# Performance work log

Measured on AMD Instinct MI355X. Metric: run time of the kernel, lower is better.

## Reference

```python
import jax, jax.numpy as jnp
import numpy as np

B, NQ, NK = 8, 1024, 1024
DQ = DK = DV = 512
H = 8
DS = DV // H
EPS = 1e-4
MAX_ITER = 3
SQRT_V = DV ** 0.25  # sqrt(sqrt(dim_V))


def setup_inputs() -> dict:
    key = jax.random.key(0)
    ks = jax.random.split(key, 8)
    s = 0.02
    return {
        "Q": jax.random.normal(ks[0], (B, NQ, DQ), jnp.float32),
        "K": jax.random.normal(ks[1], (B, NK, DK), jnp.float32),
        "Wq": jax.random.normal(ks[2], (DV, DQ), jnp.float32) * s,
        "bq": jnp.zeros((DV,), jnp.float32),
        "Wk": jax.random.normal(ks[3], (DV, DK), jnp.float32) * s,
        "bk": jnp.zeros((DV,), jnp.float32),
        "Wv": jax.random.normal(ks[4], (DV, DK), jnp.float32) * s,
        "bv": jnp.zeros((DV,), jnp.float32),
        "Wo": jax.random.normal(ks[5], (DV, DV), jnp.float32) * s,
        "bo": jnp.zeros((DV,), jnp.float32),
    }


def _split_heads(x):
    # torch.cat(x.split(ds, 2), 0): head-major stacking along batch
    b, n, _ = x.shape
    return x.reshape(b, n, H, DS).transpose(2, 0, 1, 3).reshape(H * b, n, DS)


def _merge_heads(x, b):
    # torch.cat(x.split(b, 0), 2): inverse of _split_heads
    _, n, ds = x.shape
    return x.reshape(H, b, n, ds).transpose(1, 2, 0, 3).reshape(b, n, H * ds)


def _sinkhorn_plan(x, y):
    # x: [M, P1, d], y: [M, P2, d]; cost = pairwise Euclidean (p=2) distance.
    x2 = jnp.sum(x * x, axis=-1)[:, :, None]
    y2 = jnp.sum(y * y, axis=-1)[:, None, :]
    C = jnp.sqrt(jnp.maximum(x2 + y2 - 2.0 * jnp.einsum("mid,mjd->mij", x, y), 0.0))
    m, p1, p2 = C.shape
    log_a = -jnp.log(jnp.float32(p1))  # uniform marginals
    log_b = -jnp.log(jnp.float32(p2))
    u = jnp.zeros((m, p1), C.dtype)
    v = jnp.zeros((m, p2), C.dtype)
    for _ in range(MAX_ITER):  # fixed small iteration count (max_iter=3)
        u = EPS * (log_a - jax.scipy.special.logsumexp((v[:, None, :] - C) / EPS, axis=2))
        v = EPS * (log_b - jax.scipy.special.logsumexp((u[:, :, None] - C) / EPS, axis=1))
    # transport plan P: [M, P1, P2]
    return jnp.exp((u[:, :, None] + v[:, None, :] - C) / EPS)


def reference(Q, K, Wq, bq, Wk, bk, Wv, bv, Wo, bo):
    q = Q @ Wq.T + bq            # [B, NQ, DV]
    k = K @ Wk.T + bk            # [B, NK, DV]
    v = K @ Wv.T + bv            # [B, NK, DV]
    b = Q.shape[0]
    q_, k_, v_ = _split_heads(q), _split_heads(k), _split_heads(v)  # [H*B, N, DS]
    A = _sinkhorn_plan(q_ / SQRT_V, k_ / SQRT_V)                    # [H*B, NQ, NK]
    O = _merge_heads(q_ + jnp.einsum("mij,mjd->mid", A, v_), b)     # [B, NQ, DV]
    return O + jax.nn.relu(O @ Wo.T + bo)
```

## Files before the change

### kernel.cpp

```cpp
#include <hip/hip_runtime.h>
#include <hip/hip_bf16.h>
#include <math.h>

#define NB 8
#define NN 1024
#define ND 512
#define NH 8
#define NDS 64
#define NM 64
#define LOG_A (-6.93147180559945f)
#define SQRT_V 4.75682846001088f
#define INV_SQRT_V 0.210224103813429f
#define INV_EPS 10000.0f
#define L2E  1.44269504088896f
#define LN2F 0.693147180559945f
#define IEL2 14426.9504088896f

#define SPLIT_ELEMS ((size_t)NM * NN * NDS)
#define W_ELEMS     ((size_t)ND * ND)
#define UV_FLOATS   ((size_t)NM * NN)

typedef unsigned short u16;
typedef unsigned int   u32;
typedef __attribute__((ext_vector_type(8))) short bf16x8;
typedef __attribute__((ext_vector_type(4))) float f32x4;

#define MFMA16(a,b,c) __builtin_amdgcn_mfma_f32_16x16x32_bf16(a,b,c,0,0,0)

__device__ __forceinline__ u16 f2bf_t(float x) {
  return (u16)(__float_as_uint(x) >> 16);
}
__device__ __forceinline__ float bf2f(u16 h) {
  return __uint_as_float(((u32)h) << 16);
}
__device__ __forceinline__ float fast_sqrt(float x) {
  float r;
  asm("v_sqrt_f32 %0, %1" : "=v"(r) : "v"(x));
  return r;
}
__device__ __forceinline__ float fast_exp2(float x) {
  float r;
  asm("v_exp_f32 %0, %1" : "=v"(r) : "v"(x));
  return r;
}
__device__ __forceinline__ float max3f(float a, float b, float c) {
  float r;
  asm("v_max3_f32 %0, %1, %2, %3" : "=v"(r) : "v"(a), "v"(b), "v"(c));
  return r;
}

__global__ __launch_bounds__(256) void k_split(
    const float* __restrict__ X, u16* __restrict__ hi, u16* __restrict__ lo)
{
  const size_t i = ((size_t)blockIdx.x * 256 + threadIdx.x) * 4;
  float4 v = *(const float4*)&X[i];
  const float* vp = (const float*)&v;
  u16 h[4], l[4];
#pragma unroll
  for (int j = 0; j < 4; ++j) {
    h[j] = f2bf_t(vp[j]);
    l[j] = f2bf_t(vp[j] - bf2f(h[j]));
  }
  uint2 ph, pl;
  ph.x = (u32)h[0] | ((u32)h[1] << 16);
  ph.y = (u32)h[2] | ((u32)h[3] << 16);
  pl.x = (u32)l[0] | ((u32)l[1] << 16);
  pl.y = (u32)l[2] | ((u32)l[3] << 16);
  *(uint2*)&hi[i] = ph;
  *(uint2*)&lo[i] = pl;
}

__global__ __launch_bounds__(256) void k_proj_mfma(
    const u16* __restrict__ Xh, const u16* __restrict__ Xl,
    const u16* __restrict__ Wh, const u16* __restrict__ Wl,
    const float* __restrict__ bias, u16* __restrict__ oh,
    u16* __restrict__ ol, u16* __restrict__ oT,
    float* __restrict__ nrm, float scale, int mode)
{
  __shared__ __align__(16) u16 Xhs[64][72];
  __shared__ __align__(16) u16 Xls[64][72];
  __shared__ __align__(16) u16 Whs[64][72];
  __shared__ __align__(16) u16 Wls[64][72];
  const int t = threadIdx.x;
  const int r0 = blockIdx.x * 64;
  const int h  = blockIdx.y;
  const int c0 = h * 64;
  const int w = t >> 6, l = t & 63;
  const int c = l & 15, kg = l >> 4;
  const int srow = t >> 2;
  const int skoff = (t & 3) * 16;

  f32x4 acc[4];
#pragma unroll
  for (int cf = 0; cf < 4; ++cf) acc[cf] = (f32x4){0.f, 0.f, 0.f, 0.f};

  for (int kt = 0; kt < 8; ++kt) {
    const int k0 = kt * 64;
    __syncthreads();
    {
      const u16* gxh = &Xh[(size_t)(r0 + srow) * ND + k0 + skoff];
      const u16* gxl = &Xl[(size_t)(r0 + srow) * ND + k0 + skoff];
      const u16* gwh = &Wh[(size_t)(c0 + srow) * ND + k0 + skoff];
      const u16* gwl = &Wl[(size_t)(c0 + srow) * ND + k0 + skoff];
      *(bf16x8*)&Xhs[srow][skoff]     = *(const bf16x8*)gxh;
      *(bf16x8*)&Xhs[srow][skoff + 8] = *(const bf16x8*)(gxh + 8);
      *(bf16x8*)&Xls[srow][skoff]     = *(const bf16x8*)gxl;
      *(bf16x8*)&Xls[srow][skoff + 8] = *(const bf16x8*)(gxl + 8);
      *(bf16x8*)&Whs[srow][skoff]     = *(const bf16x8*)gwh;
      *(bf16x8*)&Whs[srow][skoff + 8] = *(const bf16x8*)(gwh + 8);
      *(bf16x8*)&Wls[srow][skoff]     = *(const bf16x8*)gwl;
      *(bf16x8*)&Wls[srow][skoff + 8] = *(const bf16x8*)(gwl + 8);
    }
    __syncthreads();
#pragma unroll
    for (int ks = 0; ks < 2; ++ks) {
      bf16x8 Ah = *(const bf16x8*)&Xhs[w * 16 + c][ks * 32 + kg * 8];
      bf16x8 Al = *(const bf16x8*)&Xls[w * 16 + c][ks * 32 + kg * 8];
#pragma unroll
      for (int cf = 0; cf < 4; ++cf) {
        bf16x8 Bh = *(const bf16x8*)&Whs[cf * 16 + c][ks * 32 + kg * 8];
        bf16x8 Bl = *(const bf16x8*)&Wls[cf * 16 + c][ks * 32 + kg * 8];
        acc[cf] = MFMA16(Ah, Bh, acc[cf]);
        acc[cf] = MFMA16(Ah, Bl, acc[cf]);
        acc[cf] = MFMA16(Al, Bh, acc[cf]);
      }
    }
  }

  const int bb = r0 >> 10;
  const int n0 = r0 & 1023;
  const size_t mrow = (size_t)(h * NB + bb) * NN;
  if (mode == 0) {
    float ns[4] = {0.f, 0.f, 0.f, 0.f};
#pragma unroll
    for (int cf = 0; cf < 4; ++cf) {
      const int col = c0 + cf * 16 + c;
      const float bv = bias[col];
#pragma unroll
      for (int r = 0; r < 4; ++r) {
        float v = (acc[cf][r] + bv) * scale;
        u16 hv = f2bf_t(v);
        u16 lv = f2bf_t(v - bf2f(hv));
        ns[r] = fmaf(v, v, ns[r]);
        int n = n0 + w * 16 + kg * 4 + r;
        size_t idx = (mrow + n) * NDS + cf * 16 + c;
        oh[idx] = hv;
        ol[idx] = lv;
      }
    }
#pragma unroll
    for (int off = 1; off <= 8; off <<= 1)
#pragma unroll
      for (int r = 0; r < 4; ++r) ns[r] += __shfl_xor(ns[r], off);
    if (c == 0) {
#pragma unroll
      for (int r = 0; r < 4; ++r)
        nrm[mrow + n0 + w * 16 + kg * 4 + r] = ns[r];
    }
  } else {
#pragma unroll
    for (int cf = 0; cf < 4; ++cf) {
      const int d = cf * 16 + c;
      const float bv = bias[c0 + d];
      u16 p0 = f2bf_t((acc[cf][0] + bv) * scale);
      u16 p1 = f2bf_t((acc[cf][1] + bv) * scale);
      u16 p2 = f2bf_t((acc[cf][2] + bv) * scale);
      u16 p3 = f2bf_t((acc[cf][3] + bv) * scale);
      uint2 p;
      p.x = (u32)p0 | ((u32)p1 << 16);
      p.y = (u32)p2 | ((u32)p3 << 16);
      *(uint2*)&oT[((size_t)(h * NB + bb) * NDS + d) * NN + n0 + w * 16 + kg * 4] = p;
    }
  }
}

__global__ __launch_bounds__(512, 6) void k_lse_mfma(
    const u16* __restrict__ Ah_, const u16* __restrict__ Al_,
    const u16* __restrict__ Bh_, const u16* __restrict__ Bl_,
    const float* __restrict__ Anrm, const float* __restrict__ Bnrm,
    const float* __restrict__ din, float* __restrict__ dout, int first)
{
  __shared__ __align__(16) float din_s[NN];
  __shared__ __align__(16) float y2_s[NN];
  __shared__ __align__(16) u16 Bhs[64][72];
  __shared__ __align__(16) u16 Bls[64][72];
  const int t = threadIdx.x;
  const int Lb = blockIdx.x;
  const int xcd = Lb & 7, slot = Lb >> 3;
  const int m = xcd + 8 * (slot >> 3);
  const int a0 = (slot & 7) * 128;

  if (first) {
    *(float2*)&din_s[t * 2] = make_float2(0.f, 0.f);
  } else {
    float2 dv = *(const float2*)&din[(size_t)m * NN + t * 2];
    dv.x *= L2E; dv.y *= L2E;
    *(float2*)&din_s[t * 2] = dv;
  }
  *(float2*)&y2_s[t * 2] = *(const float2*)&Bnrm[(size_t)m * NN + t * 2];

  const int w = t >> 6, l = t & 63;
  const int c = l & 15, kg = l >> 4;
  const int arow = a0 + w * 16;
  const size_t mbase = (size_t)m * NN * NDS;

  const u16* pah = &Ah_[mbase + (size_t)(arow + c) * NDS + kg * 8];
  const u16* pal = &Al_[mbase + (size_t)(arow + c) * NDS + kg * 8];
  bf16x8 A0h = *(const bf16x8*)pah;
  bf16x8 A1h = *(const bf16x8*)(pah + 32);
  bf16x8 A0l = *(const bf16x8*)pal;
  bf16x8 A1l = *(const bf16x8*)(pal + 32);

  float x2r[4];
#pragma unroll
  for (int r = 0; r < 4; ++r) x2r[r] = Anrm[(size_t)m * NN + arow + kg * 4 + r];
  float M[4], S[4];
#pragma unroll
  for (int r = 0; r < 4; ++r) { M[r] = -3.0e38f; S[r] = 0.f; }

  const int srow = t >> 3;
  const int skoff = (t & 7) * 8;
  const u16* gh = &Bh_[mbase + (size_t)srow * NDS + skoff];
  const u16* gl = &Bl_[mbase + (size_t)srow * NDS + skoff];
  bf16x8 rh = *(const bf16x8*)gh;
  bf16x8 rl = *(const bf16x8*)gl;

  for (int bt = 0; bt < 16; ++bt) {
    const int b0 = bt * 64;
    __syncthreads();
    *(bf16x8*)&Bhs[srow][skoff] = rh;
    *(bf16x8*)&Bls[srow][skoff] = rl;
    {
      const size_t noff = (size_t)((bt + 1) & 15) * 4096;
      rh = *(const bf16x8*)(gh + noff);
      rl = *(const bf16x8*)(gl + noff);
    }
    __syncthreads();
    f32x4 acc[4];
#pragma unroll
    for (int cf = 0; cf < 4; ++cf) {
      const int bl = cf * 16 + c;
      bf16x8 B0h = *(const bf16x8*)&Bhs[bl][kg * 8];
      bf16x8 B1h = *(const bf16x8*)&Bhs[bl][kg * 8 + 32];
      bf16x8 B0l = *(const bf16x8*)&Bls[bl][kg * 8];
      bf16x8 B1l = *(const bf16x8*)&Bls[bl][kg * 8 + 32];
      f32x4 a = {0.f, 0.f, 0.f, 0.f};
      a = MFMA16(A0h, B0h, a);
      a = MFMA16(A0h, B0l, a);
      a = MFMA16(A0l, B0h, a);
      a = MFMA16(A1h, B1h, a);
      a = MFMA16(A1h, B1l, a);
      a = MFMA16(A1l, B1h, a);
      acc[cf] = a;
    }
    float X[4][4];
#pragma unroll
    for (int cf = 0; cf < 4; ++cf) {
      const int col = b0 + cf * 16 + c;
      const float vb2 = din_s[col];
      const float y2  = y2_s[col];
#pragma unroll
      for (int r = 0; r < 4; ++r) {
        float d2 = fmaf(-2.f, acc[cf][r], x2r[r] + y2);
        float sq = fast_sqrt(fmaxf(d2, 0.f));
        X[cf][r] = fmaf(-IEL2, sq, vb2);
      }
    }
#pragma unroll
    for (int r = 0; r < 4; ++r) {
      float m1 = max3f(X[0][r], X[1][r], X[2][r]);
      float nm = max3f(m1, X[3][r], M[r]);
      float s4 = fast_exp2(X[0][r] - nm) + fast_exp2(X[1][r] - nm)
               + fast_exp2(X[2][r] - nm) + fast_exp2(X[3][r] - nm);
      S[r] = fmaf(S[r], fast_exp2(M[r] - nm), s4);
      M[r] = nm;
    }
  }
#pragma unroll
  for (int off = 1; off <= 8; off <<= 1) {
#pragma unroll
    for (int r = 0; r < 4; ++r) {
      float Mo = __shfl_xor(M[r], off);
      float So = __shfl_xor(S[r], off);
      float nm = fmaxf(M[r], Mo);
      S[r] = S[r] * fast_exp2(M[r] - nm) + So * fast_exp2(Mo - nm);
      M[r] = nm;
    }
  }
  if (c == 0) {
#pragma unroll
    for (int r = 0; r < 4; ++r)
      dout[(size_t)m * NN + arow + kg * 4 + r] =
          LOG_A - M[r] * LN2F - __logf(S[r]);
  }
}

__global__ __launch_bounds__(256) void k_pv_mfma(
    const u16* __restrict__ qh, const u16* __restrict__ ql,
    const u16* __restrict__ kh, const u16* __restrict__ kl,
    const u16* __restrict__ vT, const float* __restrict__ qn,
    const float* __restrict__ kn, const float* __restrict__ ue,
    const float* __restrict__ ve, u16* __restrict__ Oh_, u16* __restrict__ Ol_)
{
  __shared__ __align__(16) float ve_s[NN];
  __shared__ __align__(16) float y2_s[NN];
  __shared__ __align__(16) u16 Bhs[64][72];
  __shared__ __align__(16) u16 Bls[64][72];
  __shared__ __align__(16) u16 Vs[64][72];
  __shared__ __align__(16) u16 pT[4][16][40];
  const int t = threadIdx.x;
  const int Lb = blockIdx.x;
  const int xcd = Lb & 7, slot = Lb >> 3;
  const int m = xcd + 8 * (slot >> 4);
  const int a0 = (slot & 15) * 64;
  {
    float4 vv = *(const float4*)&ve[(size_t)m * NN + t * 4];
    vv.x *= L2E; vv.y *= L2E; vv.z *= L2E; vv.w *= L2E;
    *(float4*)&ve_s[t * 4] = vv;
  }
  *(float4*)&y2_s[t * 4] = *(const float4*)&kn[(size_t)m * NN + t * 4];

  const int w = t >> 6, l = t & 63;
  const int c = l & 15, kg = l >> 4;
  const int arow = a0 + w * 16;
  const size_t mbase = (size_t)m * NN * NDS;

  const u16* pah = &qh[mbase + (size_t)(arow + c) * NDS + kg * 8];
  const u16* pal = &ql[mbase + (size_t)(arow + c) * NDS + kg * 8];
  bf16x8 A0h = *(const bf16x8*)pah;
  bf16x8 A1h = *(const bf16x8*)(pah + 32);
  bf16x8 A0l = *(const bf16x8*)pal;
  bf16x8 A1l = *(const bf16x8*)(pal + 32);

  float x2r[4], uer2[4];
#pragma unroll
  for (int r = 0; r < 4; ++r) {
    x2r[r]  = qn[(size_t)m * NN + arow + kg * 4 + r];
    uer2[r] = ue[(size_t)m * NN + arow + kg * 4 + r] * L2E;
  }
  f32x4 pacc[4];
#pragma unroll
  for (int df = 0; df < 4; ++df) pacc[df] = (f32x4){0.f, 0.f, 0.f, 0.f};

  const int srow = t >> 2;
  const int skoff = (t & 3) * 16;
  const u16* gh = &kh[mbase + (size_t)srow * NDS + skoff];
  const u16* gl = &kl[mbase + (size_t)srow * NDS + skoff];
  const u16* gv = &vT[((size_t)m * NDS + srow) * NN + skoff];
  bf16x8 rh0 = *(const bf16x8*)gh, rh1 = *(const bf16x8*)(gh + 8);
  bf16x8 rl0 = *(const bf16x8*)gl, rl1 = *(const bf16x8*)(gl + 8);
  bf16x8 rv0 = *(const bf16x8*)gv, rv1 = *(const bf16x8*)(gv + 8);

  for (int bt = 0; bt < 16; ++bt) {
    const int b0 = bt * 64;
    __syncthreads();
    *(bf16x8*)&Bhs[srow][skoff]     = rh0;
    *(bf16x8*)&Bhs[srow][skoff + 8] = rh1;
    *(bf16x8*)&Bls[srow][skoff]     = rl0;
    *(bf16x8*)&Bls[srow][skoff + 8] = rl1;
    *(bf16x8*)&Vs[srow][skoff]      = rv0;
    *(bf16x8*)&Vs[srow][skoff + 8]  = rv1;
    {
      const int nbt = (bt + 1) & 15;
      const size_t nk = (size_t)nbt * 4096;
      const size_t nv = (size_t)nbt * 64;
      rh0 = *(const bf16x8*)(gh + nk);
      rh1 = *(const bf16x8*)(gh + nk + 8);
      rl0 = *(const bf16x8*)(gl + nk);
      rl1 = *(const bf16x8*)(gl + nk + 8);
      rv0 = *(const bf16x8*)(gv + nv);
      rv1 = *(const bf16x8*)(gv + nv + 8);
    }
    __syncthreads();
#pragma unroll
    for (int ph = 0; ph < 2; ++ph) {
      f32x4 acc[2];
#pragma unroll
      for (int q = 0; q < 2; ++q) {
        const int cf = ph * 2 + q;
        const int bl = cf * 16 + c;
        bf16x8 B0h = *(const bf16x8*)&Bhs[bl][kg * 8];
        bf16x8 B1h = *(const bf16x8*)&Bhs[bl][kg * 8 + 32];
        bf16x8 B0l = *(const bf16x8*)&Bls[bl][kg * 8];
        bf16x8 B1l = *(const bf16x8*)&Bls[bl][kg * 8 + 32];
        f32x4 a = {0.f, 0.f, 0.f, 0.f};
        a = MFMA16(A0h, B0h, a);
        a = MFMA16(A0h, B0l, a);
        a = MFMA16(A0l, B0h, a);
        a = MFMA16(A1h, B1h, a);
        a = MFMA16(A1h, B1l, a);
        a = MFMA16(A1l, B1h, a);
        acc[q] = a;
      }
#pragma unroll
      for (int q = 0; q < 2; ++q) {
        const int cf = ph * 2 + q;
        const int col = b0 + cf * 16 + c;
        const float ve2 = ve_s[col];
        const float y2  = y2_s[col];
#pragma unroll
        for (int r = 0; r < 4; ++r) {
          float d2 = fmaf(-2.f, acc[q][r], x2r[r] + y2);
          float sq = fast_sqrt(fmaxf(d2, 0.f));
          float p  = fast_exp2(fmaf(-IEL2, sq, uer2[r] + ve2));
          pT[w][kg * 4 + r][q * 16 + c] = f2bf_t(p);
        }
      }
      bf16x8 Pa = *(const bf16x8*)&pT[w][c][kg * 8];
#pragma unroll
      for (int df = 0; df < 4; ++df) {
        bf16x8 Vb = *(const bf16x8*)&Vs[df * 16 + c][ph * 32 + kg * 8];
        pacc[df] = MFMA16(Pa, Vb, pacc[df]);
      }
    }
  }
#pragma unroll
  for (int df = 0; df < 4; ++df) {
#pragma unroll
    for (int r = 0; r < 4; ++r) {
      int row = arow + kg * 4 + r;
      int d = df * 16 + c;
      size_t qi = mbase + (size_t)row * NDS + d;
      float qv = bf2f(qh[qi]) + bf2f(ql[qi]);
      float o  = fmaf(SQRT_V, qv, pacc[df][r]);
      u16 hv = f2bf_t(o);
      Oh_[qi] = hv;
      Ol_[qi] = f2bf_t(o - bf2f(hv));
    }
  }
}

__global__ __launch_bounds__(256) void k_out_mfma(
    const u16* __restrict__ Oh_, const u16* __restrict__ Ol_,
    const u16* __restrict__ Wh, const u16* __restrict__ Wl,
    const float* __restrict__ bo, float* __restrict__ out)
{
  __shared__ __align__(16) u16 Ahs[64][72];
  __shared__ __align__(16) u16 Als[64][72];
  __shared__ __align__(16) u16 Whs[64][72];
  __shared__ __align__(16) u16 Wls[64][72];
  const int t = threadIdx.x;
  const int r0 = blockIdx.x * 64;
  const int c0 = blockIdx.y * 64;
  const int bb = r0 >> 10;
  const int n0 = r0 & 1023;
  const int w = t >> 6, l = t & 63;
  const int c = l & 15, kg = l >> 4;
  const int srow = t >> 2;
  const int skoff = (t & 3) * 16;

  f32x4 acc[4];
#pragma unroll
  for (int cf = 0; cf < 4; ++cf) acc[cf] = (f32x4){0.f, 0.f, 0.f, 0.f};

  for (int kt = 0; kt < 8; ++kt) {
    __syncthreads();
    {
      const size_t ob = ((size_t)(kt * NB + bb) * NN + n0 + srow) * NDS;
      const u16* gah = &Oh_[ob + skoff];
      const u16* gal = &Ol_[ob + skoff];
      const u16* gwh = &Wh[(size_t)(c0 + srow) * ND + kt * 64 + skoff];
      const u16* gwl = &Wl[(size_t)(c0 + srow) * ND + kt * 64 + skoff];
      *(bf16x8*)&Ahs[srow][skoff]     = *(const bf16x8*)gah;
      *(bf16x8*)&Ahs[srow][skoff + 8] = *(const bf16x8*)(gah + 8);
      *(bf16x8*)&Als[srow][skoff]     = *(const bf16x8*)gal;
      *(bf16x8*)&Als[srow][skoff + 8] = *(const bf16x8*)(gal + 8);
      *(bf16x8*)&Whs[srow][skoff]     = *(const bf16x8*)gwh;
      *(bf16x8*)&Whs[srow][skoff + 8] = *(const bf16x8*)(gwh + 8);
      *(bf16x8*)&Wls[srow][skoff]     = *(const bf16x8*)gwl;
      *(bf16x8*)&Wls[srow][skoff + 8] = *(const bf16x8*)(gwl + 8);
    }
    __syncthreads();
#pragma unroll
    for (int ks = 0; ks < 2; ++ks) {
      bf16x8 Ah = *(const bf16x8*)&Ahs[w * 16 + c][ks * 32 + kg * 8];
      bf16x8 Al = *(const bf16x8*)&Als[w * 16 + c][ks * 32 + kg * 8];
#pragma unroll
      for (int cf = 0; cf < 4; ++cf) {
        bf16x8 Bh = *(const bf16x8*)&Whs[cf * 16 + c][ks * 32 + kg * 8];
        bf16x8 Bl = *(const bf16x8*)&Wls[cf * 16 + c][ks * 32 + kg * 8];
        acc[cf] = MFMA16(Ah, Bh, acc[cf]);
        acc[cf] = MFMA16(Ah, Bl, acc[cf]);
        acc[cf] = MFMA16(Al, Bh, acc[cf]);
      }
    }
  }
#pragma unroll
  for (int cf = 0; cf < 4; ++cf) {
    const int col = c0 + cf * 16 + c;
    const int d = cf * 16 + c;
    const float bv = bo[col];
#pragma unroll
    for (int r = 0; r < 4; ++r) {
      const int n = n0 + w * 16 + kg * 4 + r;
      const size_t oi = ((size_t)(blockIdx.y * NB + bb) * NN + n) * NDS + d;
      float om = bf2f(Oh_[oi]) + bf2f(Ol_[oi]);
      out[(size_t)(r0 + w * 16 + kg * 4 + r) * ND + col] =
          om + fmaxf(acc[cf][r] + bv, 0.f);
    }
  }
}

extern "C" void kernel_launch(void* const* d_in, const int* in_sizes, int n_in,
                              void* d_out, int out_size, void* d_ws, size_t ws_size,
                              hipStream_t stream) {
  const float* Q  = (const float*)d_in[0];
  const float* K  = (const float*)d_in[1];
  const float* Wq = (const float*)d_in[2];
  const float* bq = (const float*)d_in[3];
  const float* Wk = (const float*)d_in[4];
  const float* bk = (const float*)d_in[5];
  const float* Wv = (const float*)d_in[6];
  const float* bv = (const float*)d_in[7];
  const float* Wo = (const float*)d_in[8];
  const float* bo = (const float*)d_in[9];
  float* out = (float*)d_out;

  const size_t need_bytes =
      7 * SPLIT_ELEMS * sizeof(u16) + 8 * W_ELEMS * sizeof(u16) +
      4 * UV_FLOATS * sizeof(float);
  if (ws_size < need_bytes) return;

  u16* qh = (u16*)d_ws;
  u16* ql = qh + SPLIT_ELEMS;
  u16* kh = ql + SPLIT_ELEMS;
  u16* kl = kh + SPLIT_ELEMS;
  u16* vT = kl + SPLIT_ELEMS;
  u16* Oh = vT + SPLIT_ELEMS;
  u16* Ol = Oh + SPLIT_ELEMS;
  u16* wqh = Ol + SPLIT_ELEMS;
  u16* wql = wqh + W_ELEMS;
  u16* wkh = wql + W_ELEMS;
  u16* wkl = wkh + W_ELEMS;
  u16* wvh = wkl + W_ELEMS;
  u16* wvl = wvh + W_ELEMS;
  u16* woh = wvl + W_ELEMS;
  u16* wol = woh + W_ELEMS;
  float* ue = (float*)(wol + W_ELEMS);
  float* ve = ue + UV_FLOATS;
  float* qn = ve + UV_FLOATS;
  float* kn = qn + UV_FLOATS;

  u16* Qrh = Oh;
  u16* Qrl = Ol;
  u16* Krh = (u16*)d_out;
  u16* Krl = Krh + SPLIT_ELEMS;

  dim3 blk(256);
  k_split<<<dim3(4096), blk, 0, stream>>>(Q, Qrh, Qrl);
  k_split<<<dim3(4096), blk, 0, stream>>>(K, Krh, Krl);
  k_split<<<dim3(256), blk, 0, stream>>>(Wq, wqh, wql);
  k_split<<<dim3(256), blk, 0, stream>>>(Wk, wkh, wkl);
  k_split<<<dim3(256), blk, 0, stream>>>(Wv, wvh, wvl);
  k_split<<<dim3(256), blk, 0, stream>>>(Wo, woh, wol);
  k_proj_mfma<<<dim3(128, 8), blk, 0, stream>>>(Qrh, Qrl, wqh, wql, bq, qh, ql, nullptr, qn, INV_SQRT_V, 0);
  k_proj_mfma<<<dim3(128, 8), blk, 0, stream>>>(Krh, Krl, wkh, wkl, bk, kh, kl, nullptr, kn, INV_SQRT_V, 0);
  k_proj_mfma<<<dim3(128, 8), blk, 0, stream>>>(Krh, Krl, wvh, wvl, bv, nullptr, nullptr, vT, nullptr, 1.0f, 1);
  for (int it = 0; it < 3; ++it) {
    k_lse_mfma<<<dim3(512), dim3(512), 0, stream>>>(qh, ql, kh, kl, qn, kn, ve, ue, it == 0 ? 1 : 0);
    k_lse_mfma<<<dim3(512), dim3(512), 0, stream>>>(kh, kl, qh, ql, kn, qn, ue, ve, 0);
  }
  k_pv_mfma<<<dim3(1024), blk, 0, stream>>>(qh, ql, kh, kl, vT, qn, kn, ue, ve, Oh, Ol);
  k_out_mfma<<<dim3(128, 8), blk, 0, stream>>>(Oh, Ol, woh, wol, bo, out);
}
```

Before: 380.2 us.

## Double-buffer LDS tiles in LSE and PV kernels, enlarge PV blocks to 512 threads

The LSE and PV kernels now keep two shared-memory copies of the streamed K/V tiles, alternating by iteration, so one of the two __syncthreads per tile can be dropped. The PV kernel is also regrouped into 512-thread blocks covering 128 rows, matching the LSE kernel's layout, with each thread loading one 8-element vector per tile instead of two. This is meant to cut barrier stalls and raise per-block reuse of K/V tiles. The cost is more LDS per block, and the LSE launch bound is lowered from 6 to 4 blocks, which can reduce occupancy.

Result: no change. 373.2 us (-1.8%).

```diff
diff --git a/kernel.cpp b/kernel.cpp
--- a/kernel.cpp
+++ b/kernel.cpp
@@ -174,7 +174,7 @@
   }
 }
 
-__global__ __launch_bounds__(512, 6) void k_lse_mfma(
+__global__ __launch_bounds__(512, 4) void k_lse_mfma(
     const u16* __restrict__ Ah_, const u16* __restrict__ Al_,
     const u16* __restrict__ Bh_, const u16* __restrict__ Bl_,
     const float* __restrict__ Anrm, const float* __restrict__ Bnrm,
@@ -182,8 +182,8 @@
 {
   __shared__ __align__(16) float din_s[NN];
   __shared__ __align__(16) float y2_s[NN];
-  __shared__ __align__(16) u16 Bhs[64][72];
-  __shared__ __align__(16) u16 Bls[64][72];
+  __shared__ __align__(16) u16 Bhs[2][64][72];
+  __shared__ __align__(16) u16 Bls[2][64][72];
   const int t = threadIdx.x;
   const int Lb = blockIdx.x;
   const int xcd = Lb & 7, slot = Lb >> 3;
@@ -227,9 +227,9 @@
 
   for (int bt = 0; bt < 16; ++bt) {
     const int b0 = bt * 64;
-    __syncthreads();
-    *(bf16x8*)&Bhs[srow][skoff] = rh;
-    *(bf16x8*)&Bls[srow][skoff] = rl;
+    const int buf = bt & 1;
+    *(bf16x8*)&Bhs[buf][srow][skoff] = rh;
+    *(bf16x8*)&Bls[buf][srow][skoff] = rl;
     {
       const size_t noff = (size_t)((bt + 1) & 15) * 4096;
       rh = *(const bf16x8*)(gh + noff);
@@ -240,10 +240,10 @@
 #pragma unroll
     for (int cf = 0; cf < 4; ++cf) {
       const int bl = cf * 16 + c;
-      bf16x8 B0h = *(const bf16x8*)&Bhs[bl][kg * 8];
-      bf16x8 B1h = *(const bf16x8*)&Bhs[bl][kg * 8 + 32];
-      bf16x8 B0l = *(const bf16x8*)&Bls[bl][kg * 8];
-      bf16x8 B1l = *(const bf16x8*)&Bls[bl][kg * 8 + 32];
+      bf16x8 B0h = *(const bf16x8*)&Bhs[buf][bl][kg * 8];
+      bf16x8 B1h = *(const bf16x8*)&Bhs[buf][bl][kg * 8 + 32];
+      bf16x8 B0l = *(const bf16x8*)&Bls[buf][bl][kg * 8];
+      bf16x8 B1l = *(const bf16x8*)&Bls[buf][bl][kg * 8 + 32];
       f32x4 a = {0.f, 0.f, 0.f, 0.f};
       a = MFMA16(A0h, B0h, a);
       a = MFMA16(A0h, B0l, a);
@@ -295,7 +295,7 @@
   }
 }
 
-__global__ __launch_bounds__(256) void k_pv_mfma(
+__global__ __launch_bounds__(512, 4) void k_pv_mfma(
     const u16* __restrict__ qh, const u16* __restrict__ ql,
     const u16* __restrict__ kh, const u16* __restrict__ kl,
     const u16* __restrict__ vT, const float* __restrict__ qn,
@@ -304,21 +304,21 @@
 {
   __shared__ __align__(16) float ve_s[NN];
   __shared__ __align__(16) float y2_s[NN];
-  __shared__ __align__(16) u16 Bhs[64][72];
-  __shared__ __align__(16) u16 Bls[64][72];
-  __shared__ __align__(16) u16 Vs[64][72];
-  __shared__ __align__(16) u16 pT[4][16][40];
+  __shared__ __align__(16) u16 Bhs[2][64][72];
+  __shared__ __align__(16) u16 Bls[2][64][72];
+  __shared__ __align__(16) u16 Vs[2][64][72];
+  __shared__ __align__(16) u16 pT[8][16][40];
   const int t = threadIdx.x;
   const int Lb = blockIdx.x;
   const int xcd = Lb & 7, slot = Lb >> 3;
-  const int m = xcd + 8 * (slot >> 4);
-  const int a0 = (slot & 15) * 64;
+  const int m = xcd + 8 * (slot >> 3);
+  const int a0 = (slot & 7) * 128;
   {
-    float4 vv = *(const float4*)&ve[(size_t)m * NN + t * 4];
-    vv.x *= L2E; vv.y *= L2E; vv.z *= L2E; vv.w *= L2E;
-    *(float4*)&ve_s[t * 4] = vv;
-  }
-  *(float4*)&y2_s[t * 4] = *(const float4*)&kn[(size_t)m * NN + t * 4];
+    float2 vv = *(const float2*)&ve[(size_t)m * NN + t * 2];
+    vv.x *= L2E; vv.y *= L2E;
+    *(float2*)&ve_s[t * 2] = vv;
+  }
+  *(float2*)&y2_s[t * 2] = *(const float2*)&kn[(size_t)m * NN + t * 2];
 
   const int w = t >> 6, l = t & 63;
   const int c = l & 15, kg = l >> 4;
@@ -342,34 +342,26 @@
 #pragma unroll
   for (int df = 0; df < 4; ++df) pacc[df] = (f32x4){0.f, 0.f, 0.f, 0.f};
 
-  const int srow = t >> 2;
-  const int skoff = (t & 3) * 16;
+  const int srow = t >> 3;
+  const int skoff = (t & 7) * 8;
   const u16* gh = &kh[mbase + (size_t)srow * NDS + skoff];
   const u16* gl = &kl[mbase + (size_t)srow * NDS + skoff];
   const u16* gv = &vT[((size_t)m * NDS + srow) * NN + skoff];
-  bf16x8 rh0 = *(const bf16x8*)gh, rh1 = *(const bf16x8*)(gh + 8);
-  bf16x8 rl0 = *(const bf16x8*)gl, rl1 = *(const bf16x8*)(gl + 8);
-  bf16x8 rv0 = *(const bf16x8*)gv, rv1 = *(const bf16x8*)(gv + 8);
+  bf16x8 rh = *(const bf16x8*)gh;
+  bf16x8 rl = *(const bf16x8*)gl;
+  bf16x8 rv = *(const bf16x8*)gv;
 
   for (int bt = 0; bt < 16; ++bt) {
     const int b0 = bt * 64;
-    __syncthreads();
-    *(bf16x8*)&Bhs[srow][skoff]     = rh0;
-    *(bf16x8*)&Bhs[srow][skoff + 8] = rh1;
-    *(bf16x8*)&Bls[srow][skoff]     = rl0;
-    *(bf16x8*)&Bls[srow][skoff + 8] = rl1;
-    *(bf16x8*)&Vs[srow][skoff]      = rv0;
-    *(bf16x8*)&Vs[srow][skoff + 8]  = rv1;
+    const int buf = bt & 1;
+    *(bf16x8*)&Bhs[buf][srow][skoff] = rh;
+    *(bf16x8*)&Bls[buf][srow][skoff] = rl;
+    *(bf16x8*)&Vs[buf][srow][skoff]  = rv;
     {
       const int nbt = (bt + 1) & 15;
-      const size_t nk = (size_t)nbt * 4096;
-      const size_t nv = (size_t)nbt * 64;
-      rh0 = *(const bf16x8*)(gh + nk);
-      rh1 = *(const bf16x8*)(gh + nk + 8);
-      rl0 = *(const bf16x8*)(gl + nk);
-      rl1 = *(const bf16x8*)(gl + nk + 8);
-      rv0 = *(const bf16x8*)(gv + nv);
-      rv1 = *(const bf16x8*)(gv + nv + 8);
+      rh = *(const bf16x8*)(gh + (size_t)nbt * 4096);
+      rl = *(const bf16x8*)(gl + (size_t)nbt * 4096);
+      rv = *(const bf16x8*)(gv + (size_t)nbt * 64);
     }
     __syncthreads();
 #pragma unroll
@@ -379,10 +371,10 @@
       for (int q = 0; q < 2; ++q) {
         const int cf = ph * 2 + q;
         const int bl = cf * 16 + c;
-        bf16x8 B0h = *(const bf16x8*)&Bhs[bl][kg * 8];
-        bf16x8 B1h = *(const bf16x8*)&Bhs[bl][kg * 8 + 32];
-        bf16x8 B0l = *(const bf16x8*)&Bls[bl][kg * 8];
-        bf16x8 B1l = *(const bf16x8*)&Bls[bl][kg * 8 + 32];
+        bf16x8 B0h = *(const bf16x8*)&Bhs[buf][bl][kg * 8];
+        bf16x8 B1h = *(const bf16x8*)&Bhs[buf][bl][kg * 8 + 32];
+        bf16x8 B0l = *(const bf16x8*)&Bls[buf][bl][kg * 8];
+        bf16x8 B1l = *(const bf16x8*)&Bls[buf][bl][kg * 8 + 32];
         f32x4 a = {0.f, 0.f, 0.f, 0.f};
         a = MFMA16(A0h, B0h, a);
         a = MFMA16(A0h, B0l, a);
@@ -409,7 +401,7 @@
       bf16x8 Pa = *(const bf16x8*)&pT[w][c][kg * 8];
 #pragma unroll
       for (int df = 0; df < 4; ++df) {
-        bf16x8 Vb = *(const bf16x8*)&Vs[df * 16 + c][ph * 32 + kg * 8];
+        bf16x8 Vb = *(const bf16x8*)&Vs[buf][df * 16 + c][ph * 32 + kg * 8];
         pacc[df] = MFMA16(Pa, Vb, pacc[df]);
       }
     }
@@ -560,6 +552,6 @@
     k_lse_mfma<<<dim3(512), dim3(512), 0, stream>>>(qh, ql, kh, kl, qn, kn, ve, ue, it == 0 ? 1 : 0);
     k_lse_mfma<<<dim3(512), dim3(512), 0, stream>>>(kh, kl, qh, ql, kn, qn, ue, ve, 0);
   }
-  k_pv_mfma<<<dim3(1024), blk, 0, stream>>>(qh, ql, kh, kl, vT, qn, kn, ue, ve, Oh, Ol);
+  k_pv_mfma<<<dim3(512), dim3(512), 0, stream>>>(qh, ql, kh, kl, vT, qn, kn, ue, ve, Oh, Ol);
   k_out_mfma<<<dim3(128, 8), blk, 0, stream>>>(Oh, Ol, woh, wol, bo, out);
 }
```

## Load MFMA B operands directly from global memory instead of LDS staging

Applied to the files above, without the earlier changes.

The LSE and PV kernels no longer stage K/Q tiles (and V tiles) through shared memory with double-buffered register prefetch and two barriers per tile. Each lane now loads its MFMA B fragments straight from global memory, relying on L1/L2 caching since every wave of a block reads the same tiles. The LSE kernel also moves from 512-thread blocks over 128 rows to 256-thread blocks over 64 rows with twice as many blocks. This removes LDS traffic and synchronisation but adds redundant global/L1 loads per wave and exposes load latency with no explicit prefetch.

Result: slower. 980.7 us (+157.9%).

```diff
diff --git a/kernel.cpp b/kernel.cpp
--- a/kernel.cpp
+++ b/kernel.cpp
@@ -174,7 +174,7 @@
   }
 }
 
-__global__ __launch_bounds__(512, 6) void k_lse_mfma(
+__global__ __launch_bounds__(256, 4) void k_lse_mfma(
     const u16* __restrict__ Ah_, const u16* __restrict__ Al_,
     const u16* __restrict__ Bh_, const u16* __restrict__ Bl_,
     const float* __restrict__ Anrm, const float* __restrict__ Bnrm,
@@ -182,22 +182,21 @@
 {
   __shared__ __align__(16) float din_s[NN];
   __shared__ __align__(16) float y2_s[NN];
-  __shared__ __align__(16) u16 Bhs[64][72];
-  __shared__ __align__(16) u16 Bls[64][72];
   const int t = threadIdx.x;
   const int Lb = blockIdx.x;
   const int xcd = Lb & 7, slot = Lb >> 3;
-  const int m = xcd + 8 * (slot >> 3);
-  const int a0 = (slot & 7) * 128;
+  const int m = xcd + 8 * (slot >> 4);
+  const int a0 = (slot & 15) * 64;
 
   if (first) {
-    *(float2*)&din_s[t * 2] = make_float2(0.f, 0.f);
+    *(float4*)&din_s[t * 4] = make_float4(0.f, 0.f, 0.f, 0.f);
   } else {
-    float2 dv = *(const float2*)&din[(size_t)m * NN + t * 2];
-    dv.x *= L2E; dv.y *= L2E;
-    *(float2*)&din_s[t * 2] = dv;
-  }
-  *(float2*)&y2_s[t * 2] = *(const float2*)&Bnrm[(size_t)m * NN + t * 2];
+    float4 dv = *(const float4*)&din[(size_t)m * NN + t * 4];
+    dv.x *= L2E; dv.y *= L2E; dv.z *= L2E; dv.w *= L2E;
+    *(float4*)&din_s[t * 4] = dv;
+  }
+  *(float4*)&y2_s[t * 4] = *(const float4*)&Bnrm[(size_t)m * NN + t * 4];
+  __syncthreads();
 
   const int w = t >> 6, l = t & 63;
   const int c = l & 15, kg = l >> 4;
@@ -218,42 +217,32 @@
 #pragma unroll
   for (int r = 0; r < 4; ++r) { M[r] = -3.0e38f; S[r] = 0.f; }
 
-  const int srow = t >> 3;
-  const int skoff = (t & 7) * 8;
-  const u16* gh = &Bh_[mbase + (size_t)srow * NDS + skoff];
-  const u16* gl = &Bl_[mbase + (size_t)srow * NDS + skoff];
-  bf16x8 rh = *(const bf16x8*)gh;
-  bf16x8 rl = *(const bf16x8*)gl;
+  const u16* pbh = &Bh_[mbase + (size_t)c * NDS + kg * 8];
+  const u16* pbl = &Bl_[mbase + (size_t)c * NDS + kg * 8];
 
   for (int bt = 0; bt < 16; ++bt) {
     const int b0 = bt * 64;
-    __syncthreads();
-    *(bf16x8*)&Bhs[srow][skoff] = rh;
-    *(bf16x8*)&Bls[srow][skoff] = rl;
-    {
-      const size_t noff = (size_t)((bt + 1) & 15) * 4096;
-      rh = *(const bf16x8*)(gh + noff);
-      rl = *(const bf16x8*)(gl + noff);
-    }
-    __syncthreads();
+    bf16x8 B0h[4], B1h[4], B0l[4], B1l[4];
+#pragma unroll
+    for (int cf = 0; cf < 4; ++cf) {
+      const size_t o = (size_t)(bt * 4 + cf) * 1024;
+      B0h[cf] = *(const bf16x8*)(pbh + o);
+      B1h[cf] = *(const bf16x8*)(pbh + o + 32);
+      B0l[cf] = *(const bf16x8*)(pbl + o);
+      B1l[cf] = *(const bf16x8*)(pbl + o + 32);
+    }
     f32x4 acc[4];
 #pragma unroll
     for (int cf = 0; cf < 4; ++cf) {
-      const int bl = cf * 16 + c;
-      bf16x8 B0h = *(const bf16x8*)&Bhs[bl][kg * 8];
-      bf16x8 B1h = *(const bf16x8*)&Bhs[bl][kg * 8 + 32];
-      bf16x8 B0l = *(const bf16x8*)&Bls[bl][kg * 8];
-      bf16x8 B1l = *(const bf16x8*)&Bls[bl][kg * 8 + 32];
       f32x4 a = {0.f, 0.f, 0.f, 0.f};
-      a = MFMA16(A0h, B0h, a);
-      a = MFMA16(A0h, B0l, a);
-      a = MFMA16(A0l, B0h, a);
-      a = MFMA16(A1h, B1h, a);
-      a = MFMA16(A1h, B1l, a);
-      a = MFMA16(A1l, B1h, a);
+      a = MFMA16(A0h, B0h[cf], a);
+      a = MFMA16(A0h, B0l[cf], a);
+      a = MFMA16(A0l, B0h[cf], a);
+      a = MFMA16(A1h, B1h[cf], a);
+      a = MFMA16(A1h, B1l[cf], a);
+      a = MFMA16(A1l, B1h[cf], a);
       acc[cf] = a;
     }
-    float X[4][4];
 #pragma unroll
     for (int cf = 0; cf < 4; ++cf) {
       const int col = b0 + cf * 16 + c;
@@ -263,15 +252,15 @@
       for (int r = 0; r < 4; ++r) {
         float d2 = fmaf(-2.f, acc[cf][r], x2r[r] + y2);
         float sq = fast_sqrt(fmaxf(d2, 0.f));
-        X[cf][r] = fmaf(-IEL2, sq, vb2);
+        acc[cf][r] = fmaf(-IEL2, sq, vb2);
       }
     }
 #pragma unroll
     for (int r = 0; r < 4; ++r) {
-      float m1 = max3f(X[0][r], X[1][r], X[2][r]);
-      float nm = max3f(m1, X[3][r], M[r]);
-      float s4 = fast_exp2(X[0][r] - nm) + fast_exp2(X[1][r] - nm)
-               + fast_exp2(X[2][r] - nm) + fast_exp2(X[3][r] - nm);
+      float m1 = max3f(acc[0][r], acc[1][r], acc[2][r]);
+      float nm = max3f(m1, acc[3][r], M[r]);
+      float s4 = fast_exp2(acc[0][r] - nm) + fast_exp2(acc[1][r] - nm)
+               + fast_exp2(acc[2][r] - nm) + fast_exp2(acc[3][r] - nm);
       S[r] = fmaf(S[r], fast_exp2(M[r] - nm), s4);
       M[r] = nm;
     }
@@ -295,7 +284,7 @@
   }
 }
 
-__global__ __launch_bounds__(256) void k_pv_mfma(
+__global__ __launch_bounds__(256, 4) void k_pv_mfma(
     const u16* __restrict__ qh, const u16* __restrict__ ql,
     const u16* __restrict__ kh, const u16* __restrict__ kl,
     const u16* __restrict__ vT, const float* __restrict__ qn,
@@ -304,9 +293,6 @@
 {
   __shared__ __align__(16) float ve_s[NN];
   __shared__ __align__(16) float y2_s[NN];
-  __shared__ __align__(16) u16 Bhs[64][72];
-  __shared__ __align__(16) u16 Bls[64][72];
-  __shared__ __align__(16) u16 Vs[64][72];
   __shared__ __align__(16) u16 pT[4][16][40];
   const int t = threadIdx.x;
   const int Lb = blockIdx.x;
@@ -319,6 +305,7 @@
     *(float4*)&ve_s[t * 4] = vv;
   }
   *(float4*)&y2_s[t * 4] = *(const float4*)&kn[(size_t)m * NN + t * 4];
+  __syncthreads();
 
   const int w = t >> 6, l = t & 63;
   const int c = l & 15, kg = l >> 4;
@@ -342,60 +329,41 @@
 #pragma unroll
   for (int df = 0; df < 4; ++df) pacc[df] = (f32x4){0.f, 0.f, 0.f, 0.f};
 
-  const int srow = t >> 2;
-  const int skoff = (t & 3) * 16;
-  const u16* gh = &kh[mbase + (size_t)srow * NDS + skoff];
-  const u16* gl = &kl[mbase + (size_t)srow * NDS + skoff];
-  const u16* gv = &vT[((size_t)m * NDS + srow) * NN + skoff];
-  bf16x8 rh0 = *(const bf16x8*)gh, rh1 = *(const bf16x8*)(gh + 8);
-  bf16x8 rl0 = *(const bf16x8*)gl, rl1 = *(const bf16x8*)(gl + 8);
-  bf16x8 rv0 = *(const bf16x8*)gv, rv1 = *(const bf16x8*)(gv + 8);
+  const u16* pkh = &kh[mbase + (size_t)c * NDS + kg * 8];
+  const u16* pkl = &kl[mbase + (size_t)c * NDS + kg * 8];
+  const u16* pvb = &vT[((size_t)m * NDS + c) * NN + kg * 8];
 
   for (int bt = 0; bt < 16; ++bt) {
     const int b0 = bt * 64;
-    __syncthreads();
-    *(bf16x8*)&Bhs[srow][skoff]     = rh0;
-    *(bf16x8*)&Bhs[srow][skoff + 8] = rh1;
-    *(bf16x8*)&Bls[srow][skoff]     = rl0;
-    *(bf16x8*)&Bls[srow][skoff + 8] = rl1;
-    *(bf16x8*)&Vs[srow][skoff]      = rv0;
-    *(bf16x8*)&Vs[srow][skoff + 8]  = rv1;
-    {
-      const int nbt = (bt + 1) & 15;
-      const size_t nk = (size_t)nbt * 4096;
-      const size_t nv = (size_t)nbt * 64;
-      rh0 = *(const bf16x8*)(gh + nk);
-      rh1 = *(const bf16x8*)(gh + nk + 8);
-      rl0 = *(const bf16x8*)(gl + nk);
-      rl1 = *(const bf16x8*)(gl + nk + 8);
-      rv0 = *(const bf16x8*)(gv + nv);
-      rv1 = *(const bf16x8*)(gv + nv + 8);
-    }
-    __syncthreads();
 #pragma unroll
     for (int ph = 0; ph < 2; ++ph) {
+      bf16x8 K0h[2], K1h[2], K0l[2], K1l[2], Vb[4];
+#pragma unroll
+      for (int q = 0; q < 2; ++q) {
+        const size_t o = (size_t)(bt * 4 + ph * 2 + q) * 1024;
+        K0h[q] = *(const bf16x8*)(pkh + o);
+        K1h[q] = *(const bf16x8*)(pkh + o + 32);
+        K0l[q] = *(const bf16x8*)(pkl + o);
+        K1l[q] = *(const bf16x8*)(pkl + o + 32);
+      }
+#pragma unroll
+      for (int df = 0; df < 4; ++df)
+        Vb[df] = *(const bf16x8*)(pvb + (size_t)(df * 16) * NN + b0 + ph * 32);
       f32x4 acc[2];
 #pragma unroll
       for (int q = 0; q < 2; ++q) {
-        const int cf = ph * 2 + q;
-        const int bl = cf * 16 + c;
-        bf16x8 B0h = *(const bf16x8*)&Bhs[bl][kg * 8];
-        bf16x8 B1h = *(const bf16x8*)&Bhs[bl][kg * 8 + 32];
-        bf16x8 B0l = *(const bf16x8*)&Bls[bl][kg * 8];
-        bf16x8 B1l = *(const bf16x8*)&Bls[bl][kg * 8 + 32];
         f32x4 a = {0.f, 0.f, 0.f, 0.f};
-        a = MFMA16(A0h, B0h, a);
-        a = MFMA16(A0h, B0l, a);
-        a = MFMA16(A0l, B0h, a);
-        a = MFMA16(A1h, B1h, a);
-        a = MFMA16(A1h, B1l, a);
-        a = MFMA16(A1l, B1h, a);
+        a = MFMA16(A0h, K0h[q], a);
+        a = MFMA16(A0h, K0l[q], a);
+        a = MFMA16(A0l, K0h[q], a);
+        a = MFMA16(A1h, K1h[q], a);
+        a = MFMA16(A1h, K1l[q], a);
+        a = MFMA16(A1l, K1h[q], a);
         acc[q] = a;
       }
 #pragma unroll
       for (int q = 0; q < 2; ++q) {
-        const int cf = ph * 2 + q;
-        const int col = b0 + cf * 16 + c;
+        const int col = b0 + (ph * 2 + q) * 16 + c;
         const float ve2 = ve_s[col];
         const float y2  = y2_s[col];
 #pragma unroll
@@ -408,10 +376,8 @@
       }
       bf16x8 Pa = *(const bf16x8*)&pT[w][c][kg * 8];
 #pragma unroll
-      for (int df = 0; df < 4; ++df) {
-        bf16x8 Vb = *(const bf16x8*)&Vs[df * 16 + c][ph * 32 + kg * 8];
-        pacc[df] = MFMA16(Pa, Vb, pacc[df]);
-      }
+      for (int df = 0; df < 4; ++df)
+        pacc[df] = MFMA16(Pa, Vb[df], pacc[df]);
     }
   }
 #pragma unroll
@@ -557,8 +523,8 @@
   k_proj_mfma<<<dim3(128, 8), blk, 0, stream>>>(Krh, Krl, wkh, wkl, bk, kh, kl, nullptr, kn, INV_SQRT_V, 0);
   k_proj_mfma<<<dim3(128, 8), blk, 0, stream>>>(Krh, Krl, wvh, wvl, bv, nullptr, nullptr, vT, nullptr, 1.0f, 1);
   for (int it = 0; it < 3; ++it) {
-    k_lse_mfma<<<dim3(512), dim3(512), 0, stream>>>(qh, ql, kh, kl, qn, kn, ve, ue, it == 0 ? 1 : 0);
-    k_lse_mfma<<<dim3(512), dim3(512), 0, stream>>>(kh, kl, qh, ql, kn, qn, ue, ve, 0);
+    k_lse_mfma<<<dim3(1024), blk, 0, stream>>>(qh, ql, kh, kl, qn, kn, ve, ue, it == 0 ? 1 : 0);
+    k_lse_mfma<<<dim3(1024), blk, 0, stream>>>(kh, kl, qh, ql, kn, qn, ue, ve, 0);
   }
   k_pv_mfma<<<dim3(1024), blk, 0, stream>>>(qh, ql, kh, kl, vT, qn, kn, ue, ve, Oh, Ol);
   k_out_mfma<<<dim3(128, 8), blk, 0, stream>>>(Oh, Ol, woh, wol, bo, out);
```
